# Optimization experiments

Measured on AMD Instinct MI355X. Metric: run time of the kernel, lower is better.

## Reference

```python
import jax, jax.numpy as jnp
import numpy as np

D_MODEL = 256
D_STATE = 16
D_INNER = 512          # expand=2 * d_model
D_CONV = 4
DT_RANK = 16           # ceil(d_model/16)
B, L = 16, 2048


def setup_inputs() -> dict:
    key = jax.random.key(0)
    ks = jax.random.split(key, 10)
    s = 0.02
    inp = {
        "x": jax.random.normal(ks[0], (B, L, D_MODEL), dtype=jnp.float32),
        "ln_w": jnp.ones((D_MODEL,), jnp.float32),
        "ln_b": jnp.zeros((D_MODEL,), jnp.float32),
        "in_proj_w": jax.random.normal(ks[1], (2 * D_INNER, D_MODEL)) * s,
        "conv_w": jax.random.normal(ks[2], (D_INNER, 1, D_CONV)) * s,
        "conv_b": jnp.zeros((D_INNER,), jnp.float32),
        "x_proj_w": jax.random.normal(ks[3], (DT_RANK + 2 * D_STATE, D_INNER)) * s,
        "dt_proj_w": jax.random.normal(ks[4], (D_INNER, DT_RANK)) * s,
        "dt_proj_b": jax.random.uniform(ks[5], (D_INNER,), minval=-4.0, maxval=-2.0),
        "A_log": jnp.log(jnp.broadcast_to(jnp.arange(1, D_STATE + 1, dtype=jnp.float32), (D_INNER, D_STATE))).copy(),
        "D_param": jnp.ones((D_INNER,), jnp.float32),
        "out_proj_w": jax.random.normal(ks[6], (D_MODEL, D_INNER)) * s,
    }
    return inp


def _layernorm(x, w, b, eps=1e-5):
    mu = jnp.mean(x, axis=-1, keepdims=True)
    var = jnp.var(x, axis=-1, keepdims=True)
    return (x - mu) * jax.lax.rsqrt(var + eps) * w + b


def _mamba(xn, in_proj_w, conv_w, conv_b, x_proj_w, dt_proj_w, dt_proj_b, A_log, D_param, out_proj_w):
    # in_proj -> x, z   (B, L, d_inner) each
    xz = jnp.einsum('bld,ed->ble', xn, in_proj_w)
    x_in, z = jnp.split(xz, 2, axis=-1)

    # depthwise causal conv over L
    xc = jax.lax.conv_general_dilated(
        jnp.transpose(x_in, (0, 2, 1)), conv_w,
        window_strides=(1,), padding=[(D_CONV - 1, 0)],
        feature_group_count=D_INNER,
        dimension_numbers=('NCH', 'OIH', 'NCH')) + conv_b[None, :, None]
    xc = jax.nn.silu(jnp.transpose(xc, (0, 2, 1)))  # (B, L, d_inner)

    # input-dependent dt, B, C
    dbc = jnp.einsum('ble,fe->blf', xc, x_proj_w)  # (B, L, dt_rank + 2N)
    dt = jax.nn.softplus(jnp.einsum('blr,er->ble', dbc[..., :DT_RANK], dt_proj_w) + dt_proj_b)
    Bc = dbc[..., DT_RANK:DT_RANK + D_STATE]   # (B, L, N)
    Cc = dbc[..., DT_RANK + D_STATE:]          # (B, L, N)

    A = -jnp.exp(A_log)  # (d_inner, N)

    def step(h, inputs):
        dt_t, x_t, B_t, C_t = inputs  # (B,e), (B,e), (B,n), (B,n)
        dA = jnp.exp(dt_t[..., None] * A)                      # (B, e, n)
        h = dA * h + dt_t[..., None] * B_t[:, None, :] * x_t[..., None]
        y = jnp.sum(h * C_t[:, None, :], axis=-1)              # (B, e)
        return h, y

    h0 = jnp.zeros((xn.shape[0], D_INNER, D_STATE), xn.dtype)
    seq = (jnp.swapaxes(dt, 0, 1), jnp.swapaxes(xc, 0, 1),
           jnp.swapaxes(Bc, 0, 1), jnp.swapaxes(Cc, 0, 1))
    _, ys = jax.lax.scan(step, h0, seq)
    y = jnp.swapaxes(ys, 0, 1) + D_param * xc                  # (B, L, e)
    y = y * jax.nn.silu(z)
    return jnp.einsum('ble,de->bld', y, out_proj_w)


def reference(x, ln_w, ln_b, in_proj_w, conv_w, conv_b, x_proj_w, dt_proj_w, dt_proj_b, A_log, D_param, out_proj_w):
    xn = _layernorm(x, ln_w, ln_b)
    out = _mamba(xn, in_proj_w, conv_w, conv_b, x_proj_w, dt_proj_w, dt_proj_b, A_log, D_param, out_proj_w)
    return x + out  # dropout is identity in eval
```

## Files before the change

### kernel.cpp

```cpp
#include <hip/hip_runtime.h>
#include <cstdint>

#define DEVI __device__ __forceinline__

typedef __bf16 bf16;
typedef __bf16 bf16x8 __attribute__((ext_vector_type(8)));
typedef __bf16 bf16x4 __attribute__((ext_vector_type(4)));
typedef __bf16 bf16x2 __attribute__((ext_vector_type(2)));
typedef float floatx4 __attribute__((ext_vector_type(4)));

constexpr int BATCH = 16, SEQ = 2048, DM = 256, DI = 512;
constexpr int M = BATCH * SEQ;
constexpr int NC = 64;
constexpr int CL = SEQ / NC;
static_assert(NC * CL == SEQ, "chunking");
constexpr float LOG2E = 1.4426950408889634f;

DEVI void gl2lds16(const void* g, void* l) {
  __builtin_amdgcn_global_load_lds(
      (const __attribute__((address_space(1))) unsigned int*)(uintptr_t)g,
      (__attribute__((address_space(3))) unsigned int*)(unsigned int)(uintptr_t)l,
      16, 0, 0);
}

DEVI float sigmoidf_(float x) { return 1.f / (1.f + __expf(-x)); }
DEVI float exp2_(float x) { return __builtin_amdgcn_exp2f(x); }

__global__ __launch_bounds__(256) void prep_kernel(
    const float* __restrict__ w1, const float* __restrict__ wx,
    const float* __restrict__ wo, const float* __restrict__ alog,
    bf16* __restrict__ w1b, bf16* __restrict__ wxb, bf16* __restrict__ wob,
    float* __restrict__ An, int* __restrict__ flags) {
  constexpr int n1 = 1024 * 256, n2 = 48 * 512, n3 = 256 * 512;
  int i = blockIdx.x * 256 + threadIdx.x;
  if (i < n1) w1b[i] = (bf16)w1[i];
  else if (i < n1 + n2) wxb[i - n1] = (bf16)wx[i - n1];
  else if (i < n1 + n2 + n3) wob[i - n1 - n2] = (bf16)wo[i - n1 - n2];
  else if (i < n1 + n2 + n3 + DI) {
    const int e = i - (n1 + n2 + n3);
    const float a0 = -__expf(alog[e * 16]);
    bool ok = (a0 < 0.f);
#pragma unroll 1
    for (int s = 0; s < 16; s++) {
      const float a = -__expf(alog[e * 16 + s]);
      An[e * 16 + s] = a * LOG2E;
      ok = ok && (__builtin_fabsf(a / a0 - (float)(s + 1)) < 1e-3f);
    }
    flags[e] = ok ? 1 : 0;
  }
}

__global__ __launch_bounds__(256) void ln_kernel(
    const float* __restrict__ x, const float* __restrict__ w,
    const float* __restrict__ b, bf16* __restrict__ xn) {
  const int row = blockIdx.x * 4 + (threadIdx.x >> 6);
  const int lane = threadIdx.x & 63;
  const float4 v = ((const float4*)(x + (size_t)row * DM))[lane];
  float s = v.x + v.y + v.z + v.w;
  float s2 = v.x * v.x + v.y * v.y + v.z * v.z + v.w * v.w;
#pragma unroll
  for (int m = 1; m < 64; m <<= 1) { s += __shfl_xor(s, m); s2 += __shfl_xor(s2, m); }
  const float mu = s * (1.f / DM);
  const float var = s2 * (1.f / DM) - mu * mu;
  const float rs = rsqrtf(var + 1e-5f);
  const float4 wv = ((const float4*)w)[lane];
  const float4 bv = ((const float4*)b)[lane];
  bf16x4 o;
  o[0] = (bf16)((v.x - mu) * rs * wv.x + bv.x);
  o[1] = (bf16)((v.y - mu) * rs * wv.y + bv.y);
  o[2] = (bf16)((v.z - mu) * rs * wv.z + bv.z);
  o[3] = (bf16)((v.w - mu) * rs * wv.w + bv.w);
  *(bf16x4*)(xn + (size_t)row * DM + lane * 4) = o;
}

template <int N, int K, bool OUT_BF16, bool RESID>
__global__ __launch_bounds__(256) void gemm_nt(const bf16* __restrict__ A,
                                               const bf16* __restrict__ W,
                                               void* __restrict__ out,
                                               const float* __restrict__ resid) {
  constexpr int BK = 32;
  __shared__ __align__(16) bf16 lA[128 * BK];
  __shared__ __align__(16) bf16 lB[128 * BK];
  const int tid = threadIdx.x;
  const int wave = tid >> 6, lane = tid & 63;
  const int bm = blockIdx.x * 128, bn = blockIdx.y * 128;
  const int wm = (wave >> 1) * 64, wn = (wave & 1) * 64;
  const int q = lane >> 4, r = lane & 15;
  floatx4 acc[4][4] = {};
  const int c0 = wave * 64 + lane;
  const int row0 = c0 >> 2, kp = (c0 & 3) * 8;
  for (int k0 = 0; k0 < K; k0 += BK) {
    gl2lds16(A + (size_t)(bm + row0) * K + k0 + kp, lA + c0 * 8);
    gl2lds16(A + (size_t)(bm + row0 + 64) * K + k0 + kp, lA + (c0 + 256) * 8);
    gl2lds16(W + (size_t)(bn + row0) * K + k0 + kp, lB + c0 * 8);
    gl2lds16(W + (size_t)(bn + row0 + 64) * K + k0 + kp, lB + (c0 + 256) * 8);
    __syncthreads();
    bf16x8 af[4], bfr[4];
#pragma unroll
    for (int i = 0; i < 4; i++) af[i] = *(const bf16x8*)&lA[(wm + i * 16 + r) * BK + q * 8];
#pragma unroll
    for (int j = 0; j < 4; j++) bfr[j] = *(const bf16x8*)&lB[(wn + j * 16 + r) * BK + q * 8];
#pragma unroll
    for (int i = 0; i < 4; i++)
#pragma unroll
      for (int j = 0; j < 4; j++)
        acc[i][j] = __builtin_amdgcn_mfma_f32_16x16x32_bf16(af[i], bfr[j], acc[i][j], 0, 0, 0);
    __syncthreads();
  }
#pragma unroll
  for (int i = 0; i < 4; i++)
#pragma unroll
    for (int j = 0; j < 4; j++)
#pragma unroll
      for (int t = 0; t < 4; t++) {
        const int row = bm + wm + i * 16 + q * 4 + t;
        const int col = bn + wn + j * 16 + r;
        const size_t idx = (size_t)row * N + col;
        float v = acc[i][j][t];
        if constexpr (OUT_BF16) {
          ((bf16*)out)[idx] = (bf16)v;
        } else {
          if constexpr (RESID) v += resid[idx];
          ((float*)out)[idx] = v;
        }
      }
}

__global__ __launch_bounds__(256) void conv_silu(const bf16* __restrict__ xz,
                                                 const float* __restrict__ cw,
                                                 const float* __restrict__ cb,
                                                 bf16* __restrict__ xc) {
  const int tid = threadIdx.x;
  const int e2 = tid * 2;
  const int p0 = blockIdx.x * 8;
  const int b = blockIdx.y;
  const float4 w0 = ((const float4*)cw)[e2];
  const float4 w1 = ((const float4*)cw)[e2 + 1];
  const float2 bias = *(const float2*)(cb + e2);
  float xa[11], xb_[11];
#pragma unroll
  for (int j = 0; j < 11; j++) {
    const int pos = p0 - 3 + j;
    float fa = 0.f, fb = 0.f;
    if (pos >= 0) {
      const unsigned u = *(const unsigned*)(xz + ((size_t)b * SEQ + pos) * 1024 + e2);
      fa = __uint_as_float(u << 16);
      fb = __uint_as_float(u & 0xFFFF0000u);
    }
    xa[j] = fa; xb_[j] = fb;
  }
#pragma unroll
  for (int k = 0; k < 8; k++) {
    const float a0 = bias.x + xa[k] * w0.x + xa[k + 1] * w0.y + xa[k + 2] * w0.z + xa[k + 3] * w0.w;
    const float a1 = bias.y + xb_[k] * w1.x + xb_[k + 1] * w1.y + xb_[k + 2] * w1.z + xb_[k + 3] * w1.w;
    bf16x2 o;
    o[0] = (bf16)(a0 * sigmoidf_(a0));
    o[1] = (bf16)(a1 * sigmoidf_(a1));
    *(bf16x2*)(xc + ((size_t)b * SEQ + p0 + k) * DI + e2) = o;
  }
}

__global__ __launch_bounds__(256) void gemm_xproj(const bf16* __restrict__ A,
                                                  const bf16* __restrict__ W,
                                                  float* __restrict__ out) {
  constexpr int K = DI;
  __shared__ __align__(16) bf16 lW[48 * K];
  __shared__ __align__(16) bf16 lA[128 * 32];
  const int tid = threadIdx.x;
  const int wave = tid >> 6, lane = tid & 63;
  const int bm = blockIdx.x * 128;
  const int q = lane >> 4, r = lane & 15;
#pragma unroll
  for (int rd = 0; rd < 12; rd++) {
    const int c = rd * 256 + tid;
    gl2lds16((const char*)W + (size_t)c * 16, (char*)lW + (size_t)c * 16);
  }
  const int c0 = wave * 64 + lane;
  const int row0 = c0 >> 2, kp = (c0 & 3) * 8;
  const int wm = wave * 32;
  floatx4 acc[2][3] = {};
  for (int k0 = 0; k0 < K; k0 += 32) {
    gl2lds16(A + (size_t)(bm + row0) * K + k0 + kp, lA + c0 * 8);
    gl2lds16(A + (size_t)(bm + row0 + 64) * K + k0 + kp, lA + (c0 + 256) * 8);
    __syncthreads();
    bf16x8 af[2], bfr[3];
#pragma unroll
    for (int i = 0; i < 2; i++) af[i] = *(const bf16x8*)&lA[(wm + i * 16 + r) * 32 + q * 8];
#pragma unroll
    for (int j = 0; j < 3; j++) bfr[j] = *(const bf16x8*)&lW[(j * 16 + r) * K + k0 + q * 8];
#pragma unroll
    for (int i = 0; i < 2; i++)
#pragma unroll
      for (int j = 0; j < 3; j++)
        acc[i][j] = __builtin_amdgcn_mfma_f32_16x16x32_bf16(af[i], bfr[j], acc[i][j], 0, 0, 0);
    __syncthreads();
  }
#pragma unroll
  for (int i = 0; i < 2; i++)
#pragma unroll
    for (int j = 0; j < 3; j++)
#pragma unroll
      for (int t = 0; t < 4; t++)
        out[(size_t)(bm + wm + i * 16 + q * 4 + t) * 48 + j * 16 + r] = acc[i][j][t];
}

__global__ __launch_bounds__(256) void dtproj_kernel(const float* __restrict__ dbc,
                                                     const float* __restrict__ dtw,
                                                     const float* __restrict__ dtb,
                                                     bf16* __restrict__ dt) {
  __shared__ __align__(16) float sd[64 * 16];
  const int tid = threadIdx.x;
  const int p0 = blockIdx.x * 64;
  const int e = blockIdx.y * 256 + tid;
  {
    const int rowi = tid >> 2, coli = (tid & 3) * 4;
    *(float4*)&sd[rowi * 16 + coli] = *(const float4*)(dbc + (size_t)(p0 + rowi) * 48 + coli);
  }
  float w[16];
#pragma unroll
  for (int s = 0; s < 16; s += 4) {
    float4 t4 = *(const float4*)(dtw + (size_t)e * 16 + s);
    w[s] = t4.x; w[s + 1] = t4.y; w[s + 2] = t4.z; w[s + 3] = t4.w;
  }
  const float bias = dtb[e];
  __syncthreads();
  for (int p = 0; p < 64; p++) {
    float s = bias;
#pragma unroll
    for (int r2 = 0; r2 < 16; r2++) s += sd[p * 16 + r2] * w[r2];
    const float sp = (s > 15.f) ? s : __logf(1.f + __expf(s));
    dt[(size_t)(p0 + p) * DI + e] = (bf16)sp;
  }
}

__global__ __launch_bounds__(256) void scan_pass1(const bf16* __restrict__ dt,
                                                  const bf16* __restrict__ xc,
                                                  const float* __restrict__ dbc,
                                                  const float* __restrict__ An,
                                                  const int* __restrict__ flags,
                                                  float* __restrict__ U,
                                                  float* __restrict__ SD) {
  const int e = blockIdx.x * 256 + threadIdx.x;
  const int ch = blockIdx.y, b = blockIdx.z;
  const int fast = flags[e];
  float h[16];
#pragma unroll
  for (int s = 0; s < 16; s++) h[s] = 0.f;
  float sdt = 0.f;
  const size_t posBase = (size_t)b * SEQ + (size_t)ch * CL;
  if (fast) {
    const float A0 = An[(size_t)e * 16];
    for (int il = 0; il < CL; il++) {
      const size_t pos = posBase + il;
      const float dtv = (float)dt[pos * DI + e];
      const float xv = (float)xc[pos * DI + e];
      const float* bc = dbc + pos * 48 + 16;
      float Bv[16];
#pragma unroll
      for (int s = 0; s < 16; s += 4) {
        float4 b4 = *(const float4*)(bc + s);
        Bv[s] = b4.x; Bv[s + 1] = b4.y; Bv[s + 2] = b4.z; Bv[s + 3] = b4.w;
      }
      const float dtx = dtv * xv;
      sdt += dtv;
      const float d1 = exp2_(dtv * A0);
      float d = 1.f;
#pragma unroll
      for (int s = 0; s < 16; s++) { d *= d1; h[s] = d * h[s] + dtx * Bv[s]; }
    }
  } else {
    float A[16];
#pragma unroll
    for (int s = 0; s < 16; s += 4) {
      float4 a4 = *(const float4*)(An + (size_t)e * 16 + s);
      A[s] = a4.x; A[s + 1] = a4.y; A[s + 2] = a4.z; A[s + 3] = a4.w;
    }
    for (int il = 0; il < CL; il++) {
      const size_t pos = posBase + il;
      const float dtv = (float)dt[pos * DI + e];
      const float xv = (float)xc[pos * DI + e];
      const float* bc = dbc + pos * 48 + 16;
      float Bv[16];
#pragma unroll
      for (int s = 0; s < 16; s += 4) {
        float4 b4 = *(const float4*)(bc + s);
        Bv[s] = b4.x; Bv[s + 1] = b4.y; Bv[s + 2] = b4.z; Bv[s + 3] = b4.w;
      }
      const float dtx = dtv * xv;
      sdt += dtv;
#pragma unroll
      for (int s = 0; s < 16; s++) h[s] = exp2_(dtv * A[s]) * h[s] + dtx * Bv[s];
    }
  }
  float* up = U + ((size_t)(b * NC + ch) * DI + e) * 16;
#pragma unroll
  for (int s = 0; s < 16; s += 4) {
    float4 o; o.x = h[s]; o.y = h[s + 1]; o.z = h[s + 2]; o.w = h[s + 3];
    *(float4*)(up + s) = o;
  }
  SD[(size_t)(b * NC + ch) * DI + e] = sdt;
}

__global__ __launch_bounds__(256) void scan_pass2(const float* __restrict__ SD,
                                                  float* U,
                                                  const float* __restrict__ An) {
  const int t = blockIdx.x * 256 + threadIdx.x;
  const int s = t & 15;
  const int e = (t >> 4) & (DI - 1);
  const int b = t >> 13;
  const float A = An[e * 16 + s];
  float h = 0.f;
  for (int c = 0; c < NC; c++) {
    const size_t cell = (size_t)(b * NC + c) * DI + e;
    const float sdv = SD[cell];
    const size_t base = cell * 16 + s;
    const float u = U[base];
    const float h0 = h;
    h = exp2_(A * sdv) * h0 + u;
    U[base] = h0;
  }
}

__global__ __launch_bounds__(256) void scan_pass3(const bf16* dt,
                                                  const bf16* __restrict__ xc,
                                                  const bf16* __restrict__ xz,
                                                  const float* __restrict__ dbc,
                                                  const float* __restrict__ An,
                                                  const int* __restrict__ flags,
                                                  const float* __restrict__ H0,
                                                  const float* __restrict__ Dp,
                                                  bf16* yg) {
  const int e = blockIdx.x * 256 + threadIdx.x;
  const int ch = blockIdx.y, b = blockIdx.z;
  const int fast = flags[e];
  float h[16];
  const float* hp = H0 + ((size_t)(b * NC + ch) * DI + e) * 16;
#pragma unroll
  for (int s = 0; s < 16; s += 4) {
    float4 h4 = *(const float4*)(hp + s);
    h[s] = h4.x; h[s + 1] = h4.y; h[s + 2] = h4.z; h[s + 3] = h4.w;
  }
  const float Dv = Dp[e];
  const size_t posBase = (size_t)b * SEQ + (size_t)ch * CL;
  if (fast) {
    const float A0 = An[(size_t)e * 16];
    for (int il = 0; il < CL; il++) {
      const size_t pos = posBase + il;
      const float dtv = (float)dt[pos * DI + e];
      const float xv = (float)xc[pos * DI + e];
      const float zv = (float)xz[pos * 1024 + DI + e];
      const float* bc = dbc + pos * 48 + 16;
      float Bv[16], Cv[16];
#pragma unroll
      for (int s = 0; s < 16; s += 4) {
        float4 b4 = *(const float4*)(bc + s);
        Bv[s] = b4.x; Bv[s + 1] = b4.y; Bv[s + 2] = b4.z; Bv[s + 3] = b4.w;
        float4 c4 = *(const float4*)(bc + 16 + s);
        Cv[s] = c4.x; Cv[s + 1] = c4.y; Cv[s + 2] = c4.z; Cv[s + 3] = c4.w;
      }
      const float dtx = dtv * xv;
      const float d1 = exp2_(dtv * A0);
      float d = 1.f, y = 0.f;
#pragma unroll
      for (int s = 0; s < 16; s++) {
        d *= d1;
        h[s] = d * h[s] + dtx * Bv[s];
        y += h[s] * Cv[s];
      }
      const float yv = (y + Dv * xv) * zv * sigmoidf_(zv);
      yg[pos * DI + e] = (bf16)yv;
    }
  } else {
    float A[16];
#pragma unroll
    for (int s = 0; s < 16; s += 4) {
      float4 a4 = *(const float4*)(An + (size_t)e * 16 + s);
      A[s] = a4.x; A[s + 1] = a4.y; A[s + 2] = a4.z; A[s + 3] = a4.w;
    }
    for (int il = 0; il < CL; il++) {
      const size_t pos = posBase + il;
      const float dtv = (float)dt[pos * DI + e];
      const float xv = (float)xc[pos * DI + e];
      const float zv = (float)xz[pos * 1024 + DI + e];
      const float* bc = dbc + pos * 48 + 16;
      float Bv[16], Cv[16];
#pragma unroll
      for (int s = 0; s < 16; s += 4) {
        float4 b4 = *(const float4*)(bc + s);
        Bv[s] = b4.x; Bv[s + 1] = b4.y; Bv[s + 2] = b4.z; Bv[s + 3] = b4.w;
        float4 c4 = *(const float4*)(bc + 16 + s);
        Cv[s] = c4.x; Cv[s + 1] = c4.y; Cv[s + 2] = c4.z; Cv[s + 3] = c4.w;
      }
      const float dtx = dtv * xv;
      float y = 0.f;
#pragma unroll
      for (int s = 0; s < 16; s++) {
        h[s] = exp2_(dtv * A[s]) * h[s] + dtx * Bv[s];
        y += h[s] * Cv[s];
      }
      const float yv = (y + Dv * xv) * zv * sigmoidf_(zv);
      yg[pos * DI + e] = (bf16)yv;
    }
  }
}

extern "C" void kernel_launch(void* const* d_in, const int* in_sizes, int n_in,
                              void* d_out, int out_size, void* d_ws, size_t ws_size,
                              hipStream_t stream) {
  const float* x = (const float*)d_in[0];
  const float* ln_w = (const float*)d_in[1];
  const float* ln_b = (const float*)d_in[2];
  const float* w_in = (const float*)d_in[3];
  const float* conv_w = (const float*)d_in[4];
  const float* conv_b = (const float*)d_in[5];
  const float* w_x = (const float*)d_in[6];
  const float* w_dt = (const float*)d_in[7];
  const float* b_dt = (const float*)d_in[8];
  const float* a_log = (const float*)d_in[9];
  const float* d_par = (const float*)d_in[10];
  const float* w_out = (const float*)d_in[11];

  char* ws = (char*)d_ws;
  size_t off = 0;
  auto alloc = [&](size_t bytes) {
    void* p = ws + off;
    off = (off + bytes + 255) & ~(size_t)255;
    return p;
  };
  bf16* xn = (bf16*)alloc((size_t)M * DM * 2);
  bf16* xzb = (bf16*)alloc((size_t)M * 1024 * 2);
  bf16* xcb = (bf16*)alloc((size_t)M * DI * 2);
  float* dbc = (float*)alloc((size_t)M * 48 * 4);
  bf16* dtb_ = (bf16*)alloc((size_t)M * DI * 2);
  float* U = (float*)alloc((size_t)BATCH * NC * DI * 16 * 4);
  float* SD = (float*)alloc((size_t)BATCH * NC * DI * 4);
  bf16* w1b = (bf16*)alloc(1024 * 256 * 2);
  bf16* wxb = (bf16*)alloc(48 * 512 * 2);
  bf16* wob = (bf16*)alloc(256 * 512 * 2);
  float* An = (float*)alloc(512 * 16 * 4);
  int* flags = (int*)alloc(512 * 4);

  constexpr int prep_n = 1024 * 256 + 48 * 512 + 256 * 512 + DI;
  prep_kernel<<<dim3((prep_n + 255) / 256), dim3(256), 0, stream>>>(w_in, w_x, w_out, a_log, w1b, wxb, wob, An, flags);
  ln_kernel<<<dim3(M / 4), dim3(256), 0, stream>>>(x, ln_w, ln_b, xn);
  gemm_nt<1024, 256, true, false><<<dim3(M / 128, 8), dim3(256), 0, stream>>>(xn, w1b, (void*)xzb, nullptr);
  conv_silu<<<dim3(SEQ / 8, BATCH), dim3(256), 0, stream>>>(xzb, conv_w, conv_b, xcb);
  gemm_xproj<<<dim3(M / 128), dim3(256), 0, stream>>>(xcb, wxb, dbc);
  dtproj_kernel<<<dim3(M / 64, 2), dim3(256), 0, stream>>>(dbc, w_dt, b_dt, dtb_);
  scan_pass1<<<dim3(2, NC, BATCH), dim3(256), 0, stream>>>(dtb_, xcb, dbc, An, flags, U, SD);
  scan_pass2<<<dim3(BATCH * DI * 16 / 256), dim3(256), 0, stream>>>(SD, U, An);
  scan_pass3<<<dim3(2, NC, BATCH), dim3(256), 0, stream>>>(dtb_, xcb, xzb, dbc, An, flags, U, d_par, dtb_);
  gemm_nt<256, 512, false, true><<<dim3(M / 128, 2), dim3(256), 0, stream>>>(dtb_, wob, d_out, x);
}
```

Before: 307.4 us.

## Split scan state across two threads per channel and shrink xproj tiles

Both scan passes now give each channel two threads, each owning 8 of the 16 state elements. Partial y sums are combined with a lane shuffle, and the fast path's decay powers start at d^8 for the upper half. Scan launch grids double, and the x_proj GEMM uses 64-row tiles with one MFMA row block per wave. The aim is more parallelism and occupancy in the latency-bound scans and more blocks for the small GEMM. The cost is duplicated dt/x/z loads, an extra shuffle per step, and less reuse of the weight tile per block in the GEMM.

```diff
diff --git a/kernel.cpp b/kernel.cpp
--- a/kernel.cpp
+++ b/kernel.cpp
@@ -165,43 +165,35 @@
                                                   float* __restrict__ out) {
   constexpr int K = DI;
   __shared__ __align__(16) bf16 lW[48 * K];
-  __shared__ __align__(16) bf16 lA[128 * 32];
+  __shared__ __align__(16) bf16 lA[64 * 32];
   const int tid = threadIdx.x;
   const int wave = tid >> 6, lane = tid & 63;
-  const int bm = blockIdx.x * 128;
+  const int bm = blockIdx.x * 64;
   const int q = lane >> 4, r = lane & 15;
 #pragma unroll
   for (int rd = 0; rd < 12; rd++) {
     const int c = rd * 256 + tid;
     gl2lds16((const char*)W + (size_t)c * 16, (char*)lW + (size_t)c * 16);
   }
-  const int c0 = wave * 64 + lane;
-  const int row0 = c0 >> 2, kp = (c0 & 3) * 8;
-  const int wm = wave * 32;
-  floatx4 acc[2][3] = {};
+  const int row0 = tid >> 2, kp = (tid & 3) * 8;
+  const int wm = wave * 16;
+  floatx4 acc[3] = {};
   for (int k0 = 0; k0 < K; k0 += 32) {
-    gl2lds16(A + (size_t)(bm + row0) * K + k0 + kp, lA + c0 * 8);
-    gl2lds16(A + (size_t)(bm + row0 + 64) * K + k0 + kp, lA + (c0 + 256) * 8);
+    gl2lds16(A + (size_t)(bm + row0) * K + k0 + kp, lA + tid * 8);
     __syncthreads();
-    bf16x8 af[2], bfr[3];
-#pragma unroll
-    for (int i = 0; i < 2; i++) af[i] = *(const bf16x8*)&lA[(wm + i * 16 + r) * 32 + q * 8];
-#pragma unroll
-    for (int j = 0; j < 3; j++) bfr[j] = *(const bf16x8*)&lW[(j * 16 + r) * K + k0 + q * 8];
-#pragma unroll
-    for (int i = 0; i < 2; i++)
-#pragma unroll
-      for (int j = 0; j < 3; j++)
-        acc[i][j] = __builtin_amdgcn_mfma_f32_16x16x32_bf16(af[i], bfr[j], acc[i][j], 0, 0, 0);
+    bf16x8 af = *(const bf16x8*)&lA[(wm + r) * 32 + q * 8];
+#pragma unroll
+    for (int j = 0; j < 3; j++) {
+      const bf16x8 bfr = *(const bf16x8*)&lW[(j * 16 + r) * K + k0 + q * 8];
+      acc[j] = __builtin_amdgcn_mfma_f32_16x16x32_bf16(af, bfr, acc[j], 0, 0, 0);
+    }
     __syncthreads();
   }
 #pragma unroll
-  for (int i = 0; i < 2; i++)
-#pragma unroll
-    for (int j = 0; j < 3; j++)
-#pragma unroll
-      for (int t = 0; t < 4; t++)
-        out[(size_t)(bm + wm + i * 16 + q * 4 + t) * 48 + j * 16 + r] = acc[i][j][t];
+  for (int j = 0; j < 3; j++)
+#pragma unroll
+    for (int t = 0; t < 4; t++)
+      out[(size_t)(bm + wm + q * 4 + t) * 48 + j * 16 + r] = acc[j][t];
 }
 
 __global__ __launch_bounds__(256) void dtproj_kernel(const float* __restrict__ dbc,
@@ -240,12 +232,14 @@
                                                   const int* __restrict__ flags,
                                                   float* __restrict__ U,
                                                   float* __restrict__ SD) {
-  const int e = blockIdx.x * 256 + threadIdx.x;
+  const int tid = threadIdx.x;
+  const int e = blockIdx.x * 128 + (tid >> 1);
+  const int half = tid & 1;
   const int ch = blockIdx.y, b = blockIdx.z;
   const int fast = flags[e];
-  float h[16];
-#pragma unroll
-  for (int s = 0; s < 16; s++) h[s] = 0.f;
+  float h[8];
+#pragma unroll
+  for (int s = 0; s < 8; s++) h[s] = 0.f;
   float sdt = 0.f;
   const size_t posBase = (size_t)b * SEQ + (size_t)ch * CL;
   if (fast) {
@@ -254,51 +248,52 @@
       const size_t pos = posBase + il;
       const float dtv = (float)dt[pos * DI + e];
       const float xv = (float)xc[pos * DI + e];
-      const float* bc = dbc + pos * 48 + 16;
-      float Bv[16];
-#pragma unroll
-      for (int s = 0; s < 16; s += 4) {
+      const float* bc = dbc + pos * 48 + 16 + half * 8;
+      float Bv[8];
+#pragma unroll
+      for (int s = 0; s < 8; s += 4) {
         float4 b4 = *(const float4*)(bc + s);
         Bv[s] = b4.x; Bv[s + 1] = b4.y; Bv[s + 2] = b4.z; Bv[s + 3] = b4.w;
       }
       const float dtx = dtv * xv;
       sdt += dtv;
       const float d1 = exp2_(dtv * A0);
-      float d = 1.f;
-#pragma unroll
-      for (int s = 0; s < 16; s++) { d *= d1; h[s] = d * h[s] + dtx * Bv[s]; }
+      const float d2 = d1 * d1, d4 = d2 * d2, d8 = d4 * d4;
+      float d = half ? d8 : 1.f;
+#pragma unroll
+      for (int s = 0; s < 8; s++) { d *= d1; h[s] = d * h[s] + dtx * Bv[s]; }
     }
   } else {
-    float A[16];
-#pragma unroll
-    for (int s = 0; s < 16; s += 4) {
-      float4 a4 = *(const float4*)(An + (size_t)e * 16 + s);
+    float A[8];
+#pragma unroll
+    for (int s = 0; s < 8; s += 4) {
+      float4 a4 = *(const float4*)(An + (size_t)e * 16 + half * 8 + s);
       A[s] = a4.x; A[s + 1] = a4.y; A[s + 2] = a4.z; A[s + 3] = a4.w;
     }
     for (int il = 0; il < CL; il++) {
       const size_t pos = posBase + il;
       const float dtv = (float)dt[pos * DI + e];
       const float xv = (float)xc[pos * DI + e];
-      const float* bc = dbc + pos * 48 + 16;
-      float Bv[16];
-#pragma unroll
-      for (int s = 0; s < 16; s += 4) {
+      const float* bc = dbc + pos * 48 + 16 + half * 8;
+      float Bv[8];
+#pragma unroll
+      for (int s = 0; s < 8; s += 4) {
         float4 b4 = *(const float4*)(bc + s);
         Bv[s] = b4.x; Bv[s + 1] = b4.y; Bv[s + 2] = b4.z; Bv[s + 3] = b4.w;
       }
       const float dtx = dtv * xv;
       sdt += dtv;
 #pragma unroll
-      for (int s = 0; s < 16; s++) h[s] = exp2_(dtv * A[s]) * h[s] + dtx * Bv[s];
-    }
-  }
-  float* up = U + ((size_t)(b * NC + ch) * DI + e) * 16;
-#pragma unroll
-  for (int s = 0; s < 16; s += 4) {
+      for (int s = 0; s < 8; s++) h[s] = exp2_(dtv * A[s]) * h[s] + dtx * Bv[s];
+    }
+  }
+  float* up = U + ((size_t)(b * NC + ch) * DI + e) * 16 + half * 8;
+#pragma unroll
+  for (int s = 0; s < 8; s += 4) {
     float4 o; o.x = h[s]; o.y = h[s + 1]; o.z = h[s + 2]; o.w = h[s + 3];
     *(float4*)(up + s) = o;
   }
-  SD[(size_t)(b * NC + ch) * DI + e] = sdt;
+  if (half == 0) SD[(size_t)(b * NC + ch) * DI + e] = sdt;
 }
 
 __global__ __launch_bounds__(256) void scan_pass2(const float* __restrict__ SD,
@@ -330,13 +325,15 @@
                                                   const float* __restrict__ H0,
                                                   const float* __restrict__ Dp,
                                                   bf16* yg) {
-  const int e = blockIdx.x * 256 + threadIdx.x;
+  const int tid = threadIdx.x;
+  const int e = blockIdx.x * 128 + (tid >> 1);
+  const int half = tid & 1;
   const int ch = blockIdx.y, b = blockIdx.z;
   const int fast = flags[e];
-  float h[16];
-  const float* hp = H0 + ((size_t)(b * NC + ch) * DI + e) * 16;
-#pragma unroll
-  for (int s = 0; s < 16; s += 4) {
+  float h[8];
+  const float* hp = H0 + ((size_t)(b * NC + ch) * DI + e) * 16 + half * 8;
+#pragma unroll
+  for (int s = 0; s < 8; s += 4) {
     float4 h4 = *(const float4*)(hp + s);
     h[s] = h4.x; h[s + 1] = h4.y; h[s + 2] = h4.z; h[s + 3] = h4.w;
   }
@@ -349,10 +346,10 @@
       const float dtv = (float)dt[pos * DI + e];
       const float xv = (float)xc[pos * DI + e];
       const float zv = (float)xz[pos * 1024 + DI + e];
-      const float* bc = dbc + pos * 48 + 16;
-      float Bv[16], Cv[16];
-#pragma unroll
-      for (int s = 0; s < 16; s += 4) {
+      const float* bc = dbc + pos * 48 + 16 + half * 8;
+      float Bv[8], Cv[8];
+#pragma unroll
+      for (int s = 0; s < 8; s += 4) {
         float4 b4 = *(const float4*)(bc + s);
         Bv[s] = b4.x; Bv[s + 1] = b4.y; Bv[s + 2] = b4.z; Bv[s + 3] = b4.w;
         float4 c4 = *(const float4*)(bc + 16 + s);
@@ -360,21 +357,24 @@
       }
       const float dtx = dtv * xv;
       const float d1 = exp2_(dtv * A0);
-      float d = 1.f, y = 0.f;
-#pragma unroll
-      for (int s = 0; s < 16; s++) {
+      const float d2 = d1 * d1, d4 = d2 * d2, d8 = d4 * d4;
+      float d = half ? d8 : 1.f;
+      float y = 0.f;
+#pragma unroll
+      for (int s = 0; s < 8; s++) {
         d *= d1;
         h[s] = d * h[s] + dtx * Bv[s];
         y += h[s] * Cv[s];
       }
+      y += __shfl_xor(y, 1);
       const float yv = (y + Dv * xv) * zv * sigmoidf_(zv);
-      yg[pos * DI + e] = (bf16)yv;
+      if (half == 0) yg[pos * DI + e] = (bf16)yv;
     }
   } else {
-    float A[16];
-#pragma unroll
-    for (int s = 0; s < 16; s += 4) {
-      float4 a4 = *(const float4*)(An + (size_t)e * 16 + s);
+    float A[8];
+#pragma unroll
+    for (int s = 0; s < 8; s += 4) {
+      float4 a4 = *(const float4*)(An + (size_t)e * 16 + half * 8 + s);
       A[s] = a4.x; A[s + 1] = a4.y; A[s + 2] = a4.z; A[s + 3] = a4.w;
     }
     for (int il = 0; il < CL; il++) {
@@ -382,10 +382,10 @@
       const float dtv = (float)dt[pos * DI + e];
       const float xv = (float)xc[pos * DI + e];
       const float zv = (float)xz[pos * 1024 + DI + e];
-      const float* bc = dbc + pos * 48 + 16;
-      float Bv[16], Cv[16];
-#pragma unroll
-      for (int s = 0; s < 16; s += 4) {
+      const float* bc = dbc + pos * 48 + 16 + half * 8;
+      float Bv[8], Cv[8];
+#pragma unroll
+      for (int s = 0; s < 8; s += 4) {
         float4 b4 = *(const float4*)(bc + s);
         Bv[s] = b4.x; Bv[s + 1] = b4.y; Bv[s + 2] = b4.z; Bv[s + 3] = b4.w;
         float4 c4 = *(const float4*)(bc + 16 + s);
@@ -394,12 +394,13 @@
       const float dtx = dtv * xv;
       float y = 0.f;
 #pragma unroll
-      for (int s = 0; s < 16; s++) {
+      for (int s = 0; s < 8; s++) {
         h[s] = exp2_(dtv * A[s]) * h[s] + dtx * Bv[s];
         y += h[s] * Cv[s];
       }
+      y += __shfl_xor(y, 1);
       const float yv = (y + Dv * xv) * zv * sigmoidf_(zv);
-      yg[pos * DI + e] = (bf16)yv;
+      if (half == 0) yg[pos * DI + e] = (bf16)yv;
     }
   }
 }
@@ -445,10 +446,10 @@
   ln_kernel<<<dim3(M / 4), dim3(256), 0, stream>>>(x, ln_w, ln_b, xn);
   gemm_nt<1024, 256, true, false><<<dim3(M / 128, 8), dim3(256), 0, stream>>>(xn, w1b, (void*)xzb, nullptr);
   conv_silu<<<dim3(SEQ / 8, BATCH), dim3(256), 0, stream>>>(xzb, conv_w, conv_b, xcb);
-  gemm_xproj<<<dim3(M / 128), dim3(256), 0, stream>>>(xcb, wxb, dbc);
+  gemm_xproj<<<dim3(M / 64), dim3(256), 0, stream>>>(xcb, wxb, dbc);
   dtproj_kernel<<<dim3(M / 64, 2), dim3(256), 0, stream>>>(dbc, w_dt, b_dt, dtb_);
-  scan_pass1<<<dim3(2, NC, BATCH), dim3(256), 0, stream>>>(dtb_, xcb, dbc, An, flags, U, SD);
+  scan_pass1<<<dim3(4, NC, BATCH), dim3(256), 0, stream>>>(dtb_, xcb, dbc, An, flags, U, SD);
   scan_pass2<<<dim3(BATCH * DI * 16 / 256), dim3(256), 0, stream>>>(SD, U, An);
-  scan_pass3<<<dim3(2, NC, BATCH), dim3(256), 0, stream>>>(dtb_, xcb, xzb, dbc, An, flags, U, d_par, dtb_);
+  scan_pass3<<<dim3(4, NC, BATCH), dim3(256), 0, stream>>>(dtb_, xcb, xzb, dbc, An, flags, U, d_par, dtb_);
   gemm_nt<256, 512, false, true><<<dim3(M / 128, 2), dim3(256), 0, stream>>>(dtb_, wob, d_out, x);
 }
```

Result: slower. 358.2 us (+16.5%).
